# Optimization experiments

Measured on AMD Instinct MI355X. Metric: run time of the kernel, lower is better.

Reference implementation:

```python
import jax, jax.numpy as jnp
import numpy as np

B, S, NSAMP = 64, 21, 3000
HID, SEC, N, ATT = 500, 6, 2, 128
OUT, NPROTO, NCLS, NHEAD = 128, 25, 5, 4


def _pe(length, d):
    pos = np.arange(length, dtype=np.float32)[:, None]
    div = np.exp(np.arange(0, d, 2, dtype=np.float32) * (-np.log(10000.0) / d))
    pe = np.zeros((length, d), np.float32)
    pe[:, 0::2] = np.sin(pos * div)
    pe[:, 1::2] = np.cos(pos * div)
    return jnp.asarray(pe)


def _ln(x, g, b, eps=1e-5):
    m = x.mean(-1, keepdims=True)
    v = ((x - m) ** 2).mean(-1, keepdims=True)
    return (x - m) * jax.lax.rsqrt(v + eps) * g + b


def _conv1d(x, w, b):
    y = jax.lax.conv_general_dilated(x, w, (1,), [(1, 1)], dimension_numbers=('NCH', 'OIH', 'NCH'))
    return y + b[None, :, None]


def _maxpool(x, k):
    n, c, l = x.shape
    m = (l // k) * k  # torch MaxPool1d floors
    return x[:, :, :m].reshape(n, c, l // k, k).max(-1)


def _bn_eval(x, g, b, eps=1e-5):
    # eval-mode BatchNorm1d with running_mean=0, running_var=1
    return x * (g / np.sqrt(1.0 + eps))[None, :, None] + b[None, :, None]


def setup_inputs():
    key = jax.random.key(0)
    ks = jax.random.split(key, 16)
    def w(i, shape, s=0.02):
        return jax.random.normal(ks[i], shape, jnp.float32) * s
    u = jax.random.uniform(ks[0], (B * S * N, SEC), jnp.float32, 1e-6, 1.0 - 1e-6)
    return dict(
        x=jax.random.normal(ks[1], (B, S, 1, NSAMP), jnp.float32),
        gumbel=-jnp.log(-jnp.log(u)),
        wq=w(2, (HID, ATT * N)), wk=w(3, (HID, ATT * N)),
        w1=w(4, (32, 1, 3)), b1=jnp.zeros(32), bn1_g=jnp.ones(32), bn1_b=jnp.zeros(32),
        w2=w(5, (64, 32, 3)), b2=jnp.zeros(64), bn2_g=jnp.ones(64), bn2_b=jnp.zeros(64),
        w3=w(6, (128, 64, 3)), b3=jnp.zeros(128), bn3_g=jnp.ones(128), bn3_b=jnp.zeros(128),
        fc_w=w(7, (768, 256)), fc_b=jnp.zeros(256),
        fc2_w=w(8, (256, OUT)), fc2_b=jnp.zeros(OUT),
        protos=w(9, (NPROTO, OUT), 1.0),
        in_w=w(10, (OUT, 3 * OUT)), in_b=jnp.zeros(3 * OUT),
        out_w=w(11, (OUT, OUT)), out_b=jnp.zeros(OUT),
        ln1_g=jnp.ones(OUT), ln1_b=jnp.zeros(OUT),
        ln2_g=jnp.ones(OUT), ln2_b=jnp.zeros(OUT),
        ff1_w=w(12, (OUT, OUT)), ff1_b=jnp.zeros(OUT),
        ff2_w=w(13, (OUT, OUT)), ff2_b=jnp.zeros(OUT),
        clf_w=w(14, (OUT, NCLS)), clf_b=jnp.zeros(NCLS),
    )


def reference(x, gumbel, wq, wk, w1, b1, bn1_g, bn1_b, w2, b2, bn2_g, bn2_b,
              w3, b3, bn3_g, bn3_b, fc_w, fc_b, fc2_w, fc2_b, protos,
              in_w, in_b, out_w, out_b, ln1_g, ln1_b, ln2_g, ln2_b,
              ff1_w, ff1_b, ff2_w, ff2_b, clf_w, clf_b):
    bs = B * S
    # ---- HardAttentionLayer (gumbel hard sampling over SEC sections) ----
    xr = x.reshape(bs, SEC, HID)                       # (BS, 6, 500)
    xp = xr + _pe(100, HID)[None, :SEC]
    q = (xp @ wq).reshape(bs, SEC, N, ATT).transpose(0, 2, 1, 3)  # bnsh
    k = (xp @ wk).reshape(bs, SEC, N, ATT).transpose(0, 2, 1, 3)
    att = jnp.einsum('bnsh,bnth->bnst', q, k) / (HID ** 0.5)
    logits = (att.sum(-1) / SEC).reshape(bs * N, SEC)
    y_soft = jax.nn.softmax(logits + gumbel)           # tau = 1.0
    y_hard = jax.nn.one_hot(jnp.argmax(y_soft, -1), SEC, dtype=y_soft.dtype)
    alphas = (y_hard - jax.lax.stop_gradient(y_soft) + y_soft).reshape(bs, N, SEC)
    sampled = jnp.einsum('bns,bsh->bnh', alphas, xr)   # (BS, N, 500)
    # ---- conv/MLP epoch encoder (eval: dropout off, BN running stats) ----
    c = sampled.reshape(bs * N, 1, HID)
    c = _bn_eval(_maxpool(jax.nn.relu(_conv1d(c, w1, b1)), 4), bn1_g, bn1_b)
    c = _bn_eval(_maxpool(jax.nn.relu(_conv1d(c, w2, b2)), HID // 100), bn2_g, bn2_b)
    c = _bn_eval(_maxpool(jax.nn.relu(_conv1d(c, w3, b3)), 4), bn3_g, bn3_b)
    c = c.reshape(bs * N, -1) @ fc_w + fc_b
    z = c @ fc2_w + fc2_b                              # (B*S*N, 128)
    # ---- PrototypeLayer: VQ codebook lookup with straight-through ----
    d2 = (z * z).sum(1, keepdims=True) + (protos * protos).sum(1) - 2.0 * z @ protos.T
    proto = protos[jnp.argmin(d2, 1)]
    proto_st = z + jax.lax.stop_gradient(proto - z)
    # ---- SequenceEncoder: 1-layer post-norm transformer ----
    p_clf = proto_st.reshape(B, S, N, OUT).sum(2) / N  # (B, S, 128)
    h = p_clf + _pe(1024, OUT)[None, :S]
    qkv = h @ in_w + in_b
    qh, kh, vh = [t.reshape(B, S, NHEAD, OUT // NHEAD) for t in jnp.split(qkv, 3, -1)]
    sc = jnp.einsum('bqhd,bkhd->bhqk', qh, kh) / ((OUT // NHEAD) ** 0.5)
    ctx = jnp.einsum('bhqk,bkhd->bqhd', jax.nn.softmax(sc, -1), vh).reshape(B, S, OUT)
    h = _ln(h + ctx @ out_w + out_b, ln1_g, ln1_b)
    ff = jax.nn.relu(h @ ff1_w + ff1_b) @ ff2_w + ff2_b
    h = _ln(h + ff, ln2_g, ln2_b)
    return (h.reshape(-1, OUT) @ clf_w + clf_b).reshape(B, S, NCLS)
```

## Files before the change

kernel.cpp:

```cpp
#include <hip/hip_runtime.h>
#include <math.h>

#define BB 64
#define SS 21
#define NSAMP 3000
#define HID 500
#define SECN 6
#define NN 2
#define OUTD 128
#define NPROTO 25
#define NCLS 5
#define NHEAD 4
#define BS (BB*SS)
#define NSAMPLE (BS*NN)

#define C500 (-0.0184206807439523674f)
#define C128 (-0.07195578415606439f)
#define LSCALE 0.00745355992499929898f

#define WS_W2HI 5376
#define WS_W2LO 8448
#define WS_W3HI 11520
#define WS_W3LO 23808
#define WS_P3   36096
#define WS_C3   55296
#define WS_WQT  55424
#define WS_V    727424
#define WS_QKV  WS_V
#define WS_CTX  (WS_V + 520192)

typedef __attribute__((ext_vector_type(8))) short short8;
typedef __attribute__((ext_vector_type(4))) float floatx4;

__device__ __forceinline__ short f2bf(float f) {
  unsigned u = __float_as_uint(f);
  u += 0x7FFF + ((u >> 16) & 1);
  return (short)(u >> 16);
}
__device__ __forceinline__ float bf2f(short h) {
  return __uint_as_float(((unsigned)(unsigned short)h) << 16);
}

__global__ __launch_bounds__(256) void prep_all_kernel(
    const float* __restrict__ w2, const float* __restrict__ w3,
    short* __restrict__ w2hi, short* __restrict__ w2lo,
    short* __restrict__ w3hi, short* __restrict__ w3lo,
    const float* __restrict__ protos, const float* __restrict__ fc2w,
    const float* __restrict__ fcw, const float* __restrict__ fcb,
    const float* __restrict__ fc2b,
    float* __restrict__ P3, float* __restrict__ c3,
    const float* __restrict__ wq, float* __restrict__ wqT) {
  __shared__ __align__(16) float p2row[256];
  __shared__ float red[256];
  __shared__ float tile[64][65];
  const int t = threadIdx.x;
  if (blockIdx.x < 120) {
    int idx = blockIdx.x * 256 + t;
    if (idx < 6144) {
      int ic = idx & 31, ck = idx >> 5, k = ck % 3, c = ck / 3;
      float v = w2[c * 96 + ic * 3 + k];
      int dst = (((k * 4 + (c >> 4)) * 64) + ((ic >> 3) * 16 + (c & 15))) * 8 + (ic & 7);
      short hi = f2bf(v);
      short lo = f2bf(v - bf2f(hi));
      w2hi[dst] = hi; w2lo[dst] = lo;
    } else if (idx < 30720) {
      int j = idx - 6144;
      int ic = j & 63, ck = j >> 6, k = ck % 3, c = ck / 3;
      float v = w3[(c * 64 + ic) * 3 + k];
      int s = k * 2 + (ic >> 5);
      int dst = (((s * 8 + (c >> 4)) * 64) + (((ic & 31) >> 3) * 16 + (c & 15))) * 8 + (ic & 7);
      short hi = f2bf(v);
      short lo = f2bf(v - bf2f(hi));
      w3hi[dst] = hi; w3lo[dst] = lo;
    }
    return;
  }
  if (blockIdx.x >= 145) {
    int tid = blockIdx.x - 145;
    int h0 = (tid >> 2) * 64, c0 = (tid & 3) * 64;
    for (int e = t; e < 4096; e += 256) {
      int i = e >> 6, j = e & 63;
      if (h0 + i < 500) tile[j][i] = wq[(h0 + i) * 256 + c0 + j];
    }
    __syncthreads();
    for (int e = t; e < 4096; e += 256) {
      int c = e >> 6, hh = e & 63;
      if (h0 + hh < 500) wqT[(c0 + c) * 500 + h0 + hh] = tile[c][hh];
    }
    return;
  }
  const int p = blockIdx.x - 120, j = t;
  {
    const float4* pr = reinterpret_cast<const float4*>(protos + p * 128);
    const float4* wr = reinterpret_cast<const float4*>(fc2w + j * 128);
    float4 a4 = make_float4(0.f, 0.f, 0.f, 0.f);
    for (int c4 = 0; c4 < 32; c4++) {
      float4 a = pr[c4], b = wr[c4];
      a4.x += a.x * b.x; a4.y += a.y * b.y; a4.z += a.z * b.z; a4.w += a.w * b.w;
    }
    float v = (a4.x + a4.y) + (a4.z + a4.w);
    p2row[j] = v;
    float contrib = v * fcb[j];
    if (j < 128) {
      float pv = protos[p * 128 + j];
      contrib += pv * fc2b[j] - 0.5f * pv * pv;
    }
    red[j] = contrib;
  }
  __syncthreads();
  for (int s = 128; s > 0; s >>= 1) {
    if (j < s) red[j] += red[j + s];
    __syncthreads();
  }
  if (j == 0) c3[p] = red[0];
  for (int k = j; k < 768; k += 256) {
    const float4* fr = reinterpret_cast<const float4*>(fcw + k * 256);
    const float4* p2 = reinterpret_cast<const float4*>(p2row);
    float4 a4 = make_float4(0.f, 0.f, 0.f, 0.f);
    for (int j4 = 0; j4 < 64; j4++) {
      float4 a = p2[j4], b = fr[j4];
      a4.x += a.x * b.x; a4.y += a.y * b.y; a4.z += a.z * b.z; a4.w += a.w * b.w;
    }
    P3[p * 768 + k] = (a4.x + a4.y) + (a4.z + a4.w);
  }
}

#define MBX 4
__global__ __launch_bounds__(512) void attn_b_kernel(
    const float* __restrict__ x, const float* __restrict__ wk,
    const float* __restrict__ wqT, float* __restrict__ v) {
  __shared__ __align__(16) float pesum[500];
  __shared__ __align__(16) float xs[MBX * 500];
  __shared__ __align__(16) float ksp[2 * 256 * MBX];
  __shared__ __align__(16) float ks_t[256 * MBX];
  const int blk = blockIdx.x, t = threadIdx.x;

  if (t < 125) {
    float div0 = expf((float)(4 * t) * C500);
    float div1 = expf((float)(4 * t + 2) * C500);
    float s0 = 0.f, c0 = 0.f, s1 = 0.f, c1 = 0.f;
#pragma unroll
    for (int s = 0; s < SECN; s++) {
      float a0 = (float)s * div0, a1 = (float)s * div1;
      s0 += sinf(a0); c0 += cosf(a0);
      s1 += sinf(a1); c1 += cosf(a1);
    }
    reinterpret_cast<float4*>(pesum)[t] = make_float4(s0, c0, s1, c1);
  }
  __syncthreads();

  for (int e = t; e < MBX * 125; e += 512) {
    int m = e / 125, h4 = e % 125;
    const float4* xr = reinterpret_cast<const float4*>(x) + (blk * MBX + m) * 750;
    float4 a = xr[h4];
#pragma unroll
    for (int s = 1; s < SECN; s++) {
      float4 b = xr[s * 125 + h4];
      a.x += b.x; a.y += b.y; a.z += b.z; a.w += b.w;
    }
    float4 pe = reinterpret_cast<float4*>(pesum)[h4];
    a.x += pe.x; a.y += pe.y; a.z += pe.z; a.w += pe.w;
    reinterpret_cast<float4*>(xs)[m * 125 + h4] = a;
  }
  __syncthreads();

  {
    int c = t & 255, kh = t >> 8;
    float acc[MBX];
#pragma unroll
    for (int m = 0; m < MBX; m++) acc[m] = 0.f;
    int b4 = kh ? 63 : 0, e4 = kh ? 125 : 63;
    const float4* xsb = reinterpret_cast<const float4*>(xs);
    for (int i4 = b4; i4 < e4; i4++) {
      int i = i4 * 4;
      float w0 = wk[(i + 0) * 256 + c];
      float w1 = wk[(i + 1) * 256 + c];
      float w2 = wk[(i + 2) * 256 + c];
      float w3 = wk[(i + 3) * 256 + c];
#pragma unroll
      for (int m = 0; m < MBX; m++) {
        float4 xv = xsb[m * 125 + i4];
        acc[m] += xv.x * w0 + xv.y * w1 + xv.z * w2 + xv.w * w3;
      }
    }
#pragma unroll
    for (int m = 0; m < MBX; m++)
      ksp[(kh * 256 + c) * MBX + m] = acc[m];
  }
  __syncthreads();
  for (int e = t; e < 256 * MBX; e += 512) ks_t[e] = ksp[e] + ksp[256 * MBX + e];
  __syncthreads();

  if (t < 500) {
    int h = t;
#pragma unroll
    for (int n = 0; n < 2; n++) {
      float acc[MBX];
#pragma unroll
      for (int m = 0; m < MBX; m++) acc[m] = 0.f;
      const float* wcol = wqT + (n * 128) * 500 + h;
      const floatx4* ktb = (const floatx4*)ks_t + n * 128;
      for (int c = 0; c < 128; c++) {
        float w = wcol[c * 500];
        floatx4 k0 = ktb[c];
        acc[0] += w * k0[0]; acc[1] += w * k0[1]; acc[2] += w * k0[2]; acc[3] += w * k0[3];
      }
#pragma unroll
      for (int m = 0; m < MBX; m++)
        v[((blk * MBX + m) * 2 + n) * 500 + h] = acc[m];
    }
  }
}

__global__ __launch_bounds__(192) void attn_c_kernel(
    const float* __restrict__ x, const float* __restrict__ v,
    const float* __restrict__ gumbel, int* __restrict__ sec_idx) {
  __shared__ float lgsh[NN][SECN];
  const int bs = blockIdx.x, t = threadIdx.x;
  const int s = t >> 5, lane = t & 31;
  const float4* x4 = reinterpret_cast<const float4*>(x) + bs * 750 + s * 125;
  const float4* v0 = reinterpret_cast<const float4*>(v) + bs * 250;
  const float4* v1 = v0 + 125;
  float a0 = 0.f, a1 = 0.f;
  for (int h4 = lane; h4 < 125; h4 += 32) {
    float4 xv = x4[h4];
    float div0 = expf((float)(4 * h4) * C500);
    float div1 = expf((float)(4 * h4 + 2) * C500);
    float ang0 = (float)s * div0, ang1 = (float)s * div1;
    xv.x += sinf(ang0); xv.y += cosf(ang0);
    xv.z += sinf(ang1); xv.w += cosf(ang1);
    float4 w0 = v0[h4], w1 = v1[h4];
    a0 += xv.x * w0.x + xv.y * w0.y + xv.z * w0.z + xv.w * w0.w;
    a1 += xv.x * w1.x + xv.y * w1.y + xv.z * w1.z + xv.w * w1.w;
  }
#pragma unroll
  for (int m = 16; m >= 1; m >>= 1) {
    a0 += __shfl_xor(a0, m);
    a1 += __shfl_xor(a1, m);
  }
  if (lane == 0) {
    lgsh[0][s] = a0 * LSCALE + gumbel[(bs * 2 + 0) * SECN + s];
    lgsh[1][s] = a1 * LSCALE + gumbel[(bs * 2 + 1) * SECN + s];
  }
  __syncthreads();
  if (t < 2) {
    int best = 0; float bv = lgsh[t][0];
    for (int i = 1; i < SECN; i++) {
      float q = lgsh[t][i];
      if (q > bv) { bv = q; best = i; }
    }
    sec_idx[bs * 2 + t] = best;
  }
}

#define CONV_LDS 53568
__global__ __launch_bounds__(512, 6) void conv_kernel(
    const float* __restrict__ x, const int* __restrict__ sec_idx,
    const float* __restrict__ w1, const float* __restrict__ b1,
    const float* __restrict__ bn1g, const float* __restrict__ bn1b,
    const short* __restrict__ w2hi, const short* __restrict__ w2lo,
    const float* __restrict__ b2,
    const float* __restrict__ bn2g, const float* __restrict__ bn2b,
    const short* __restrict__ w3hi, const short* __restrict__ w3lo,
    const float* __restrict__ b3,
    const float* __restrict__ bn3g, const float* __restrict__ bn3b,
    const float* __restrict__ P3, const float* __restrict__ c3,
    int* __restrict__ proto_idx) {
  __shared__ __align__(16) char smem[CONV_LDS];
  short* act1_hi  = (short*)smem;
  short* act1_lo  = (short*)(smem + 10400);
  short* act2p_hi = (short*)smem;
  short* act2p_lo = (short*)(smem + 4896);
  float* featsh   = (float*)(smem + 9792);
  float* sc25     = (float*)(smem + 12864);
  float* in0p  = (float*)(smem + 20800);
  float* act2t = (float*)(smem + 20800);
  float* act3t = (float*)(smem + 20800);

  const int sample = blockIdx.x;
  const int t = threadIdx.x;
  const int bsIdx = sample >> 1;
  const float bnscale = rsqrtf(1.0f + 1e-5f);
  const int wv = t >> 6, l = t & 63, lr = l & 15, lg2 = l >> 4;

  {
    int sec = sec_idx[sample];
    const float* src = &x[bsIdx * NSAMP + sec * HID];
    if (t < 512) in0p[t] = (t >= 1 && t <= 500) ? src[t - 1] : 0.f;
    if (t < 200) {
      int r = t / 40; r = (r == 0) ? 0 : 125 + r;
      int idx = r * 40 + t % 40;
      act1_hi[idx] = 0; act1_lo[idx] = 0;
    }
  }
  __syncthreads();

  {
    int ic = t & 31;
    float w0 = w1[ic * 3], w1v = w1[ic * 3 + 1], w2v = w1[ic * 3 + 2];
    float bb = b1[ic];
    float g = bn1g[ic] * bnscale, be = bn1b[ic];
    for (int p = t >> 5; p < 125; p += 16) {
      int base = 4 * p;
      float xm1 = in0p[base], x0 = in0p[base + 1], x1 = in0p[base + 2],
            x2 = in0p[base + 3], x3 = in0p[base + 4], x4 = in0p[base + 5];
      float a0 = bb + w0 * xm1 + w1v * x0 + w2v * x1;
      float a1 = bb + w0 * x0  + w1v * x1 + w2v * x2;
      float a2 = bb + w0 * x1  + w1v * x2 + w2v * x3;
      float a3 = bb + w0 * x2  + w1v * x3 + w2v * x4;
      float m = fmaxf(fmaxf(fmaxf(fmaxf(a0, a1), a2), a3), 0.f);
      float v = m * g + be;
      short hi = f2bf(v);
      short lo = f2bf(v - bf2f(hi));
      act1_hi[(p + 1) * 40 + ic] = hi;
      act1_lo[(p + 1) * 40 + ic] = lo;
    }
  }
  __syncthreads();

  {
    floatx4 acc[4];
#pragma unroll
    for (int m = 0; m < 4; m++) acc[m] = (floatx4){0.f, 0.f, 0.f, 0.f};
#pragma unroll
    for (int s = 0; s < 3; s++) {
      short8 Ah[4], Al[4], Bh, Bl;
#pragma unroll
      for (int m = 0; m < 4; m++) {
        int aoff = ((s * 4 + m) * 64 + l) * 8;
        Ah[m] = *(const short8*)(w2hi + aoff);
        Al[m] = *(const short8*)(w2lo + aoff);
      }
      {
        int boff = (wv * 16 + lr + s) * 40 + lg2 * 8;
        Bh = *(const short8*)(act1_hi + boff);
        Bl = *(const short8*)(act1_lo + boff);
      }
#pragma unroll
      for (int m = 0; m < 4; m++) {
        acc[m] = __builtin_amdgcn_mfma_f32_16x16x32_bf16(Ah[m], Bh, acc[m], 0, 0, 0);
        acc[m] = __builtin_amdgcn_mfma_f32_16x16x32_bf16(Ah[m], Bl, acc[m], 0, 0, 0);
        acc[m] = __builtin_amdgcn_mfma_f32_16x16x32_bf16(Al[m], Bh, acc[m], 0, 0, 0);
      }
    }
#pragma unroll
    for (int m = 0; m < 4; m++) {
      int p = wv * 16 + lr;
      int swz = (m * 4 + lg2) ^ lr;
      *(floatx4*)(act2t + p * 64 + swz * 4) = acc[m];
    }
  }
  __syncthreads();

  {
    if (t < 162) {
      for (int i = t; i < 648; i += 162) {
        int r = i / 72; r = (r == 0) ? 0 : 25 + r;
        int idx = r * 72 + i % 72;
        act2p_hi[idx] = 0; act2p_lo[idx] = 0;
      }
    }
    int ic = t & 63;
    float bb = b2[ic], g = bn2g[ic] * bnscale, be = bn2b[ic];
#define A2T(r, c) act2t[(r) * 64 + ((((c) >> 2) ^ ((r) & 15)) << 2) + ((c) & 3)]
    for (int pw = t >> 6; pw < 25; pw += 8) {
      int base = 5 * pw;
      float m = A2T(base, ic);
      m = fmaxf(m, A2T(base + 1, ic));
      m = fmaxf(m, A2T(base + 2, ic));
      m = fmaxf(m, A2T(base + 3, ic));
      m = fmaxf(m, A2T(base + 4, ic));
      float v = fmaxf(m + bb, 0.f) * g + be;
      short hi = f2bf(v);
      short lo = f2bf(v - bf2f(hi));
      act2p_hi[(pw + 1) * 72 + ic] = hi;
      act2p_lo[(pw + 1) * 72 + ic] = lo;
    }
#undef A2T
  }
  __syncthreads();

  {
    floatx4 acc[2];
#pragma unroll
    for (int nn = 0; nn < 2; nn++) acc[nn] = (floatx4){0.f, 0.f, 0.f, 0.f};
#pragma unroll
    for (int s = 0; s < 6; s++) {
      short8 Ah, Al, Bh[2], Bl[2];
      {
        int aoff = ((s * 8 + wv) * 64 + l) * 8;
        Ah = *(const short8*)(w3hi + aoff);
        Al = *(const short8*)(w3lo + aoff);
      }
#pragma unroll
      for (int nn = 0; nn < 2; nn++) {
        int boff = (nn * 16 + lr + (s >> 1)) * 72 + (s & 1) * 32 + lg2 * 8;
        Bh[nn] = *(const short8*)(act2p_hi + boff);
        Bl[nn] = *(const short8*)(act2p_lo + boff);
      }
#pragma unroll
      for (int nn = 0; nn < 2; nn++) {
        acc[nn] = __builtin_amdgcn_mfma_f32_16x16x32_bf16(Ah, Bh[nn], acc[nn], 0, 0, 0);
        acc[nn] = __builtin_amdgcn_mfma_f32_16x16x32_bf16(Ah, Bl[nn], acc[nn], 0, 0, 0);
        acc[nn] = __builtin_amdgcn_mfma_f32_16x16x32_bf16(Al, Bh[nn], acc[nn], 0, 0, 0);
      }
    }
#pragma unroll
    for (int nn = 0; nn < 2; nn++) {
      int p = nn * 16 + lr;
      *(floatx4*)(act3t + p * 132 + wv * 16 + lg2 * 4) = acc[nn];
    }
  }
  __syncthreads();

  {
    int c = t & 127;
    float bb = b3[c], g = bn3g[c] * bnscale, be = bn3b[c];
    for (int pw = t >> 7; pw < 6; pw += 4) {
      int base = 4 * pw;
      float m = act3t[base * 132 + c];
      m = fmaxf(m, act3t[(base + 1) * 132 + c]);
      m = fmaxf(m, act3t[(base + 2) * 132 + c]);
      m = fmaxf(m, act3t[(base + 3) * 132 + c]);
      float v = fmaxf(m + bb, 0.f) * g + be;
      featsh[c * 6 + pw] = v;
    }
  }
  __syncthreads();

  if (t < NPROTO * 8) {
    int p = t >> 3, part = t & 7;
    const float4* pr = reinterpret_cast<const float4*>(P3 + p * 768 + part * 96);
    const float4* fr = reinterpret_cast<const float4*>(featsh + part * 96);
    float4 a4 = make_float4(0.f, 0.f, 0.f, 0.f);
#pragma unroll
    for (int i = 0; i < 24; i++) {
      float4 w = pr[i], f = fr[i];
      a4.x += w.x * f.x; a4.y += w.y * f.y; a4.z += w.z * f.z; a4.w += w.w * f.w;
    }
    float a = (a4.x + a4.y) + (a4.z + a4.w);
    a += __shfl_xor(a, 1);
    a += __shfl_xor(a, 2);
    a += __shfl_xor(a, 4);
    if (part == 0) sc25[p] = a + c3[p];
  }
  __syncthreads();
  if (t == 0) {
    int best = 0; float bv = sc25[0];
    for (int i = 1; i < NPROTO; i++) {
      float v = sc25[i];
      if (v > bv) { bv = v; best = i; }
    }
    proto_idx[sample] = best;
  }
}

__global__ __launch_bounds__(384) void seq_qkv_kernel(
    const int* __restrict__ proto_idx, const float* __restrict__ protos,
    const float* __restrict__ inw, const float* __restrict__ inb,
    float* __restrict__ qkv) {
  __shared__ __align__(16) float hrow[OUTD];
  const int bs = blockIdx.x, t = threadIdx.x;
  const int s = bs % SS;
  if (t < OUTD) {
    int i0 = proto_idx[bs * 2], i1 = proto_idx[bs * 2 + 1];
    float pc = 0.5f * (protos[i0 * OUTD + t] + protos[i1 * OUTD + t]);
    float div = expf((float)(2 * (t >> 1)) * C128);
    float ang = (float)s * div;
    float pe = (t & 1) ? cosf(ang) : sinf(ang);
    hrow[t] = pc + pe;
  }
  __syncthreads();
  float a = inb[t];
  const float4* hr = reinterpret_cast<const float4*>(hrow);
  for (int d4 = 0; d4 < 32; d4++) {
    float4 h4 = hr[d4];
    int d = d4 * 4;
    a += h4.x * inw[(d + 0) * 384 + t] + h4.y * inw[(d + 1) * 384 + t]
       + h4.z * inw[(d + 2) * 384 + t] + h4.w * inw[(d + 3) * 384 + t];
  }
  qkv[bs * 384 + t] = a;
}

__global__ __launch_bounds__(256) void seq_attn_kernel(
    const float* __restrict__ qkv, float* __restrict__ ctxbuf) {
  __shared__ float qs_[SS][32], ks_[SS][32], vs_[SS][32];
  __shared__ float sc_[SS][SS + 1];
  const int b = blockIdx.x >> 2, hd = blockIdx.x & 3;
  const int t = threadIdx.x;
  for (int e = t; e < SS * 32; e += 256) {
    int s = e >> 5, dd = e & 31;
    const float* base = qkv + (b * SS + s) * 384 + hd * 32 + dd;
    qs_[s][dd] = base[0];
    ks_[s][dd] = base[128];
    vs_[s][dd] = base[256];
  }
  __syncthreads();
  for (int e = t; e < SS * SS; e += 256) {
    int qs = e / SS, ks = e % SS;
    float a = 0.f;
#pragma unroll
    for (int d = 0; d < 32; d++) a += qs_[qs][d] * ks_[ks][d];
    sc_[qs][ks] = a * 0.17677669529663689f;
  }
  __syncthreads();
  if (t < SS) {
    float mx = sc_[t][0];
    for (int i = 1; i < SS; i++) mx = fmaxf(mx, sc_[t][i]);
    float sum = 0.f;
    for (int i = 0; i < SS; i++) { float e = expf(sc_[t][i] - mx); sc_[t][i] = e; sum += e; }
    float inv = 1.f / sum;
    for (int i = 0; i < SS; i++) sc_[t][i] *= inv;
  }
  __syncthreads();
  for (int e = t; e < SS * 32; e += 256) {
    int qs = e >> 5, dd = e & 31;
    float a = 0.f;
#pragma unroll
    for (int ks = 0; ks < SS; ks++) a += sc_[qs][ks] * vs_[ks][dd];
    ctxbuf[(b * SS + qs) * OUTD + hd * 32 + dd] = a;
  }
}

__global__ __launch_bounds__(128) void seq_tail_kernel(
    const int* __restrict__ proto_idx, const float* __restrict__ protos,
    const float* __restrict__ ctxbuf,
    const float* __restrict__ outw, const float* __restrict__ outb,
    const float* __restrict__ ln1g, const float* __restrict__ ln1b,
    const float* __restrict__ ff1w, const float* __restrict__ ff1b,
    const float* __restrict__ ff2w, const float* __restrict__ ff2b,
    const float* __restrict__ ln2g, const float* __restrict__ ln2b,
    const float* __restrict__ clfw, const float* __restrict__ clfb,
    float* __restrict__ out) {
  __shared__ __align__(16) float rowA[OUTD];
  __shared__ __align__(16) float rowB[OUTD];
  __shared__ float lds2[2];
  const int bs = blockIdx.x, t = threadIdx.x;
  const int s = bs % SS;

  rowA[t] = ctxbuf[bs * OUTD + t];
  __syncthreads();
  float a = outb[t];
  {
    const float4* cr = reinterpret_cast<const float4*>(rowA);
    for (int e4 = 0; e4 < 32; e4++) {
      float4 c4 = cr[e4];
      int e = e4 * 4;
      a += c4.x * outw[(e + 0) * OUTD + t] + c4.y * outw[(e + 1) * OUTD + t]
         + c4.z * outw[(e + 2) * OUTD + t] + c4.w * outw[(e + 3) * OUTD + t];
    }
  }
  float hv;
  {
    int i0 = proto_idx[bs * 2], i1 = proto_idx[bs * 2 + 1];
    float pc = 0.5f * (protos[i0 * OUTD + t] + protos[i1 * OUTD + t]);
    float div = expf((float)(2 * (t >> 1)) * C128);
    float ang = (float)s * div;
    float pe = (t & 1) ? cosf(ang) : sinf(ang);
    hv = pc + pe;
  }
  float tmp = hv + a;
  {
    float v = tmp;
#pragma unroll
    for (int k = 32; k >= 1; k >>= 1) v += __shfl_xor(v, k);
    if ((t & 63) == 0) lds2[t >> 6] = v;
    __syncthreads();
    float m = (lds2[0] + lds2[1]) * (1.0f / OUTD);
    __syncthreads();
    float u = tmp - m;
    float w = u * u;
#pragma unroll
    for (int k = 32; k >= 1; k >>= 1) w += __shfl_xor(w, k);
    if ((t & 63) == 0) lds2[t >> 6] = w;
    __syncthreads();
    float var = (lds2[0] + lds2[1]) * (1.0f / OUTD);
    __syncthreads();
    rowA[t] = u * rsqrtf(var + 1e-5f) * ln1g[t] + ln1b[t];
  }
  __syncthreads();
  {
    float r = ff1b[t];
    const float4* hr = reinterpret_cast<const float4*>(rowA);
    for (int e4 = 0; e4 < 32; e4++) {
      float4 h4 = hr[e4];
      int e = e4 * 4;
      r += h4.x * ff1w[(e + 0) * OUTD + t] + h4.y * ff1w[(e + 1) * OUTD + t]
         + h4.z * ff1w[(e + 2) * OUTD + t] + h4.w * ff1w[(e + 3) * OUTD + t];
    }
    rowB[t] = fmaxf(r, 0.f);
  }
  __syncthreads();
  float tmp2;
  {
    float r = ff2b[t];
    const float4* cr = reinterpret_cast<const float4*>(rowB);
    for (int e4 = 0; e4 < 32; e4++) {
      float4 c4 = cr[e4];
      int e = e4 * 4;
      r += c4.x * ff2w[(e + 0) * OUTD + t] + c4.y * ff2w[(e + 1) * OUTD + t]
         + c4.z * ff2w[(e + 2) * OUTD + t] + c4.w * ff2w[(e + 3) * OUTD + t];
    }
    tmp2 = rowA[t] + r;
  }
  __syncthreads();
  {
    float v = tmp2;
#pragma unroll
    for (int k = 32; k >= 1; k >>= 1) v += __shfl_xor(v, k);
    if ((t & 63) == 0) lds2[t >> 6] = v;
    __syncthreads();
    float m = (lds2[0] + lds2[1]) * (1.0f / OUTD);
    __syncthreads();
    float u = tmp2 - m;
    float w = u * u;
#pragma unroll
    for (int k = 32; k >= 1; k >>= 1) w += __shfl_xor(w, k);
    if ((t & 63) == 0) lds2[t >> 6] = w;
    __syncthreads();
    float var = (lds2[0] + lds2[1]) * (1.0f / OUTD);
    rowA[t] = u * rsqrtf(var + 1e-5f) * ln2g[t] + ln2b[t];
  }
  __syncthreads();
  if (t < NCLS) {
    float acc = clfb[t];
    for (int d = 0; d < OUTD; d++) acc += rowA[d] * clfw[d * NCLS + t];
    out[bs * NCLS + t] = acc;
  }
}

extern "C" void kernel_launch(void* const* d_in, const int* in_sizes, int n_in,
                              void* d_out, int out_size, void* d_ws, size_t ws_size,
                              hipStream_t stream) {
  const float* x     = (const float*)d_in[0];
  const float* gum   = (const float*)d_in[1];
  const float* wq    = (const float*)d_in[2];
  const float* wk    = (const float*)d_in[3];
  const float* w1    = (const float*)d_in[4];
  const float* b1    = (const float*)d_in[5];
  const float* bn1g  = (const float*)d_in[6];
  const float* bn1b  = (const float*)d_in[7];
  const float* w2    = (const float*)d_in[8];
  const float* b2    = (const float*)d_in[9];
  const float* bn2g  = (const float*)d_in[10];
  const float* bn2b  = (const float*)d_in[11];
  const float* w3    = (const float*)d_in[12];
  const float* b3    = (const float*)d_in[13];
  const float* bn3g  = (const float*)d_in[14];
  const float* bn3b  = (const float*)d_in[15];
  const float* fcw   = (const float*)d_in[16];
  const float* fcb   = (const float*)d_in[17];
  const float* fc2w  = (const float*)d_in[18];
  const float* fc2b  = (const float*)d_in[19];
  const float* prot  = (const float*)d_in[20];
  const float* inw   = (const float*)d_in[21];
  const float* inb   = (const float*)d_in[22];
  const float* outw  = (const float*)d_in[23];
  const float* outb  = (const float*)d_in[24];
  const float* ln1g  = (const float*)d_in[25];
  const float* ln1b  = (const float*)d_in[26];
  const float* ln2g  = (const float*)d_in[27];
  const float* ln2b  = (const float*)d_in[28];
  const float* ff1w  = (const float*)d_in[29];
  const float* ff1b  = (const float*)d_in[30];
  const float* ff2w  = (const float*)d_in[31];
  const float* ff2b  = (const float*)d_in[32];
  const float* clfw  = (const float*)d_in[33];
  const float* clfb  = (const float*)d_in[34];
  float* out = (float*)d_out;

  int* sec_idx   = (int*)d_ws;
  int* proto_idx = sec_idx + NSAMPLE;
  short* w2hi = (short*)((float*)d_ws + WS_W2HI);
  short* w2lo = (short*)((float*)d_ws + WS_W2LO);
  short* w3hi = (short*)((float*)d_ws + WS_W3HI);
  short* w3lo = (short*)((float*)d_ws + WS_W3LO);
  float* P3   = (float*)d_ws + WS_P3;
  float* c3   = (float*)d_ws + WS_C3;
  float* wqT  = (float*)d_ws + WS_WQT;
  float* vbuf = (float*)d_ws + WS_V;
  float* qkv  = (float*)d_ws + WS_QKV;
  float* ctxb = (float*)d_ws + WS_CTX;

  hipLaunchKernelGGL(prep_all_kernel, dim3(177), dim3(256), 0, stream,
                     w2, w3, w2hi, w2lo, w3hi, w3lo,
                     prot, fc2w, fcw, fcb, fc2b, P3, c3, wq, wqT);
  hipLaunchKernelGGL(attn_b_kernel, dim3(BS / MBX), dim3(512), 0, stream,
                     x, wk, wqT, vbuf);
  hipLaunchKernelGGL(attn_c_kernel, dim3(BS), dim3(192), 0, stream,
                     x, vbuf, gum, sec_idx);
  hipLaunchKernelGGL(conv_kernel, dim3(NSAMPLE), dim3(512), 0, stream,
                     x, sec_idx, w1, b1, bn1g, bn1b, w2hi, w2lo, b2, bn2g, bn2b,
                     w3hi, w3lo, b3, bn3g, bn3b, P3, c3, proto_idx);
  hipLaunchKernelGGL(seq_qkv_kernel, dim3(BS), dim3(384), 0, stream,
                     proto_idx, prot, inw, inb, qkv);
  hipLaunchKernelGGL(seq_attn_kernel, dim3(BB * NHEAD), dim3(256), 0, stream,
                     qkv, ctxb);
  hipLaunchKernelGGL(seq_tail_kernel, dim3(BS), dim3(128), 0, stream,
                     proto_idx, prot, ctxb, outw, outb, ln1g, ln1b,
                     ff1w, ff1b, ff2w, ff2b, ln2g, ln2b, clfw, clfb, out);
}
```

Baseline: 183.1 us.

## Restructure kernel pipeline: fuse prep into attention, fuse QKV into seq attention, repad conv LDS

The weight prep and prototype-projection work moves into the attention-scoring kernel as extra blocks, with only the wq transpose kept as its own small launch. The sequence QKV projection is fused into the per-head attention kernel, so the qkv buffer round trip and one launch go away, though each head block recomputes its whole h row. The conv kernel's act2 LDS row stride changes from 72 to 68 shorts to reduce bank conflicts, and 8-wide loads are split into pairs of 4-wide loads. Its occupancy hint in launch bounds drops from 6 to 3, which may raise register use per thread.

```diff
diff --git a/kernel.cpp b/kernel.cpp
--- a/kernel.cpp
+++ b/kernel.cpp
@@ -26,10 +26,10 @@
 #define WS_C3   55296
 #define WS_WQT  55424
 #define WS_V    727424
-#define WS_QKV  WS_V
 #define WS_CTX  (WS_V + 520192)
 
 typedef __attribute__((ext_vector_type(8))) short short8;
+typedef __attribute__((ext_vector_type(4))) short short4v;
 typedef __attribute__((ext_vector_type(4))) float floatx4;
 
 __device__ __forceinline__ short f2bf(float f) {
@@ -41,99 +41,103 @@
   return __uint_as_float(((unsigned)(unsigned short)h) << 16);
 }
 
-__global__ __launch_bounds__(256) void prep_all_kernel(
+__global__ __launch_bounds__(256) void transpose_kernel(
+    const float* __restrict__ wq, float* __restrict__ wqT) {
+  __shared__ float tile[64][65];
+  const int t = threadIdx.x;
+  int h0 = (blockIdx.x >> 2) * 64, c0 = (blockIdx.x & 3) * 64;
+  for (int e = t; e < 4096; e += 256) {
+    int i = e >> 6, j = e & 63;
+    if (h0 + i < 500) tile[j][i] = wq[(h0 + i) * 256 + c0 + j];
+  }
+  __syncthreads();
+  for (int e = t; e < 4096; e += 256) {
+    int c = e >> 6, hh = e & 63;
+    if (h0 + hh < 500) wqT[(c0 + c) * 500 + h0 + hh] = tile[c][hh];
+  }
+}
+
+#define MBX 4
+__global__ __launch_bounds__(512) void attn_prep_kernel(
+    const float* __restrict__ x, const float* __restrict__ wk,
+    const float* __restrict__ wqT, float* __restrict__ v,
     const float* __restrict__ w2, const float* __restrict__ w3,
     short* __restrict__ w2hi, short* __restrict__ w2lo,
     short* __restrict__ w3hi, short* __restrict__ w3lo,
     const float* __restrict__ protos, const float* __restrict__ fc2w,
     const float* __restrict__ fcw, const float* __restrict__ fcb,
     const float* __restrict__ fc2b,
-    float* __restrict__ P3, float* __restrict__ c3,
-    const float* __restrict__ wq, float* __restrict__ wqT) {
-  __shared__ __align__(16) float p2row[256];
-  __shared__ float red[256];
-  __shared__ float tile[64][65];
+    float* __restrict__ P3, float* __restrict__ c3) {
   const int t = threadIdx.x;
-  if (blockIdx.x < 120) {
-    int idx = blockIdx.x * 256 + t;
-    if (idx < 6144) {
-      int ic = idx & 31, ck = idx >> 5, k = ck % 3, c = ck / 3;
-      float v = w2[c * 96 + ic * 3 + k];
-      int dst = (((k * 4 + (c >> 4)) * 64) + ((ic >> 3) * 16 + (c & 15))) * 8 + (ic & 7);
-      short hi = f2bf(v);
-      short lo = f2bf(v - bf2f(hi));
-      w2hi[dst] = hi; w2lo[dst] = lo;
-    } else if (idx < 30720) {
-      int j = idx - 6144;
-      int ic = j & 63, ck = j >> 6, k = ck % 3, c = ck / 3;
-      float v = w3[(c * 64 + ic) * 3 + k];
-      int s = k * 2 + (ic >> 5);
-      int dst = (((s * 8 + (c >> 4)) * 64) + (((ic & 31) >> 3) * 16 + (c & 15))) * 8 + (ic & 7);
-      short hi = f2bf(v);
-      short lo = f2bf(v - bf2f(hi));
-      w3hi[dst] = hi; w3lo[dst] = lo;
+  if (blockIdx.x >= 336) {
+    int pid = blockIdx.x - 336;
+    if (pid < 120) {
+      if (t < 256) {
+        int idx = pid * 256 + t;
+        if (idx < 6144) {
+          int ic = idx & 31, ck = idx >> 5, k = ck % 3, c = ck / 3;
+          float vv = w2[c * 96 + ic * 3 + k];
+          int dst = (((k * 4 + (c >> 4)) * 64) + ((ic >> 3) * 16 + (c & 15))) * 8 + (ic & 7);
+          short hi = f2bf(vv);
+          short lo = f2bf(vv - bf2f(hi));
+          w2hi[dst] = hi; w2lo[dst] = lo;
+        } else if (idx < 30720) {
+          int j = idx - 6144;
+          int ic = j & 63, ck = j >> 6, k = ck % 3, c = ck / 3;
+          float vv = w3[(c * 64 + ic) * 3 + k];
+          int s = k * 2 + (ic >> 5);
+          int dst = (((s * 8 + (c >> 4)) * 64) + (((ic & 31) >> 3) * 16 + (c & 15))) * 8 + (ic & 7);
+          short hi = f2bf(vv);
+          short lo = f2bf(vv - bf2f(hi));
+          w3hi[dst] = hi; w3lo[dst] = lo;
+        }
+      }
+      return;
+    }
+    __shared__ __align__(16) float p2row[256];
+    __shared__ float red[256];
+    const int p = pid - 120, j = t;
+    if (j < 256) {
+      const float4* pr = reinterpret_cast<const float4*>(protos + p * 128);
+      const float4* wr = reinterpret_cast<const float4*>(fc2w + j * 128);
+      float4 a4 = make_float4(0.f, 0.f, 0.f, 0.f);
+      for (int c4 = 0; c4 < 32; c4++) {
+        float4 a = pr[c4], b = wr[c4];
+        a4.x += a.x * b.x; a4.y += a.y * b.y; a4.z += a.z * b.z; a4.w += a.w * b.w;
+      }
+      float vv = (a4.x + a4.y) + (a4.z + a4.w);
+      p2row[j] = vv;
+      float contrib = vv * fcb[j];
+      if (j < 128) {
+        float pv = protos[p * 128 + j];
+        contrib += pv * fc2b[j] - 0.5f * pv * pv;
+      }
+      red[j] = contrib;
+    }
+    __syncthreads();
+    for (int s = 128; s > 0; s >>= 1) {
+      if (j < s) red[j] += red[j + s];
+      __syncthreads();
+    }
+    if (j == 0) c3[p] = red[0];
+    for (int k = t; k < 768; k += 512) {
+      const float4* fr = reinterpret_cast<const float4*>(fcw + k * 256);
+      const float4* p2 = reinterpret_cast<const float4*>(p2row);
+      float4 a4 = make_float4(0.f, 0.f, 0.f, 0.f);
+      for (int j4 = 0; j4 < 64; j4++) {
+        float4 a = p2[j4], b = fr[j4];
+        a4.x += a.x * b.x; a4.y += a.y * b.y; a4.z += a.z * b.z; a4.w += a.w * b.w;
+      }
+      P3[p * 768 + k] = (a4.x + a4.y) + (a4.z + a4.w);
     }
     return;
   }
-  if (blockIdx.x >= 145) {
-    int tid = blockIdx.x - 145;
-    int h0 = (tid >> 2) * 64, c0 = (tid & 3) * 64;
-    for (int e = t; e < 4096; e += 256) {
-      int i = e >> 6, j = e & 63;
-      if (h0 + i < 500) tile[j][i] = wq[(h0 + i) * 256 + c0 + j];
-    }
-    __syncthreads();
-    for (int e = t; e < 4096; e += 256) {
-      int c = e >> 6, hh = e & 63;
-      if (h0 + hh < 500) wqT[(c0 + c) * 500 + h0 + hh] = tile[c][hh];
-    }
-    return;
-  }
-  const int p = blockIdx.x - 120, j = t;
-  {
-    const float4* pr = reinterpret_cast<const float4*>(protos + p * 128);
-    const float4* wr = reinterpret_cast<const float4*>(fc2w + j * 128);
-    float4 a4 = make_float4(0.f, 0.f, 0.f, 0.f);
-    for (int c4 = 0; c4 < 32; c4++) {
-      float4 a = pr[c4], b = wr[c4];
-      a4.x += a.x * b.x; a4.y += a.y * b.y; a4.z += a.z * b.z; a4.w += a.w * b.w;
-    }
-    float v = (a4.x + a4.y) + (a4.z + a4.w);
-    p2row[j] = v;
-    float contrib = v * fcb[j];
-    if (j < 128) {
-      float pv = protos[p * 128 + j];
-      contrib += pv * fc2b[j] - 0.5f * pv * pv;
-    }
-    red[j] = contrib;
-  }
-  __syncthreads();
-  for (int s = 128; s > 0; s >>= 1) {
-    if (j < s) red[j] += red[j + s];
-    __syncthreads();
-  }
-  if (j == 0) c3[p] = red[0];
-  for (int k = j; k < 768; k += 256) {
-    const float4* fr = reinterpret_cast<const float4*>(fcw + k * 256);
-    const float4* p2 = reinterpret_cast<const float4*>(p2row);
-    float4 a4 = make_float4(0.f, 0.f, 0.f, 0.f);
-    for (int j4 = 0; j4 < 64; j4++) {
-      float4 a = p2[j4], b = fr[j4];
-      a4.x += a.x * b.x; a4.y += a.y * b.y; a4.z += a.z * b.z; a4.w += a.w * b.w;
-    }
-    P3[p * 768 + k] = (a4.x + a4.y) + (a4.z + a4.w);
-  }
-}
-
-#define MBX 4
-__global__ __launch_bounds__(512) void attn_b_kernel(
-    const float* __restrict__ x, const float* __restrict__ wk,
-    const float* __restrict__ wqT, float* __restrict__ v) {
+
   __shared__ __align__(16) float pesum[500];
   __shared__ __align__(16) float xs[MBX * 500];
   __shared__ __align__(16) float ksp[2 * 256 * MBX];
   __shared__ __align__(16) float ks_t[256 * MBX];
-  const int blk = blockIdx.x, t = threadIdx.x;
+  const int blk = blockIdx.x;
 
   if (t < 125) {
     float div0 = expf((float)(4 * t) * C500);
@@ -175,12 +179,12 @@
       int i = i4 * 4;
       float w0 = wk[(i + 0) * 256 + c];
       float w1 = wk[(i + 1) * 256 + c];
-      float w2 = wk[(i + 2) * 256 + c];
-      float w3 = wk[(i + 3) * 256 + c];
+      float w2v = wk[(i + 2) * 256 + c];
+      float w3v = wk[(i + 3) * 256 + c];
 #pragma unroll
       for (int m = 0; m < MBX; m++) {
         float4 xv = xsb[m * 125 + i4];
-        acc[m] += xv.x * w0 + xv.y * w1 + xv.z * w2 + xv.w * w3;
+        acc[m] += xv.x * w0 + xv.y * w1 + xv.z * w2v + xv.w * w3v;
       }
     }
 #pragma unroll
@@ -254,7 +258,8 @@
 }
 
 #define CONV_LDS 53568
-__global__ __launch_bounds__(512, 6) void conv_kernel(
+#define ST2P 68
+__global__ __launch_bounds__(512, 3) void conv_kernel(
     const float* __restrict__ x, const int* __restrict__ sec_idx,
     const float* __restrict__ w1, const float* __restrict__ b1,
     const float* __restrict__ bn1g, const float* __restrict__ bn1b,
@@ -270,7 +275,7 @@
   short* act1_hi  = (short*)smem;
   short* act1_lo  = (short*)(smem + 10400);
   short* act2p_hi = (short*)smem;
-  short* act2p_lo = (short*)(smem + 4896);
+  short* act2p_lo = (short*)(smem + 4624);
   float* featsh   = (float*)(smem + 9792);
   float* sc25     = (float*)(smem + 12864);
   float* in0p  = (float*)(smem + 20800);
@@ -353,10 +358,10 @@
   __syncthreads();
 
   {
-    if (t < 162) {
-      for (int i = t; i < 648; i += 162) {
-        int r = i / 72; r = (r == 0) ? 0 : 25 + r;
-        int idx = r * 72 + i % 72;
+    if (t < 153) {
+      for (int i = t; i < 612; i += 153) {
+        int r = i / ST2P; r = (r == 0) ? 0 : 25 + r;
+        int idx = r * ST2P + i % ST2P;
         act2p_hi[idx] = 0; act2p_lo[idx] = 0;
       }
     }
@@ -373,8 +378,8 @@
       float v = fmaxf(m + bb, 0.f) * g + be;
       short hi = f2bf(v);
       short lo = f2bf(v - bf2f(hi));
-      act2p_hi[(pw + 1) * 72 + ic] = hi;
-      act2p_lo[(pw + 1) * 72 + ic] = lo;
+      act2p_hi[(pw + 1) * ST2P + ic] = hi;
+      act2p_lo[(pw + 1) * ST2P + ic] = lo;
     }
 #undef A2T
   }
@@ -394,9 +399,13 @@
       }
 #pragma unroll
       for (int nn = 0; nn < 2; nn++) {
-        int boff = (nn * 16 + lr + (s >> 1)) * 72 + (s & 1) * 32 + lg2 * 8;
-        Bh[nn] = *(const short8*)(act2p_hi + boff);
-        Bl[nn] = *(const short8*)(act2p_lo + boff);
+        int boff = (nn * 16 + lr + (s >> 1)) * ST2P + (s & 1) * 32 + lg2 * 8;
+        short4v h0 = *(const short4v*)(act2p_hi + boff);
+        short4v h1 = *(const short4v*)(act2p_hi + boff + 4);
+        short4v l0 = *(const short4v*)(act2p_lo + boff);
+        short4v l1 = *(const short4v*)(act2p_lo + boff + 4);
+        Bh[nn] = (short8){h0[0], h0[1], h0[2], h0[3], h1[0], h1[1], h1[2], h1[3]};
+        Bl[nn] = (short8){l0[0], l0[1], l0[2], l0[3], l1[0], l1[1], l1[2], l1[3]};
       }
 #pragma unroll
       for (int nn = 0; nn < 2; nn++) {
@@ -455,47 +464,46 @@
   }
 }
 
-__global__ __launch_bounds__(384) void seq_qkv_kernel(
+__global__ __launch_bounds__(256) void seq_qk_attn_kernel(
     const int* __restrict__ proto_idx, const float* __restrict__ protos,
     const float* __restrict__ inw, const float* __restrict__ inb,
-    float* __restrict__ qkv) {
-  __shared__ __align__(16) float hrow[OUTD];
-  const int bs = blockIdx.x, t = threadIdx.x;
-  const int s = bs % SS;
-  if (t < OUTD) {
-    int i0 = proto_idx[bs * 2], i1 = proto_idx[bs * 2 + 1];
-    float pc = 0.5f * (protos[i0 * OUTD + t] + protos[i1 * OUTD + t]);
-    float div = expf((float)(2 * (t >> 1)) * C128);
-    float ang = (float)s * div;
-    float pe = (t & 1) ? cosf(ang) : sinf(ang);
-    hrow[t] = pc + pe;
-  }
-  __syncthreads();
-  float a = inb[t];
-  const float4* hr = reinterpret_cast<const float4*>(hrow);
-  for (int d4 = 0; d4 < 32; d4++) {
-    float4 h4 = hr[d4];
-    int d = d4 * 4;
-    a += h4.x * inw[(d + 0) * 384 + t] + h4.y * inw[(d + 1) * 384 + t]
-       + h4.z * inw[(d + 2) * 384 + t] + h4.w * inw[(d + 3) * 384 + t];
-  }
-  qkv[bs * 384 + t] = a;
-}
-
-__global__ __launch_bounds__(256) void seq_attn_kernel(
-    const float* __restrict__ qkv, float* __restrict__ ctxbuf) {
+    float* __restrict__ ctxbuf) {
+  __shared__ __align__(16) float hsh[SS * OUTD];
   __shared__ float qs_[SS][32], ks_[SS][32], vs_[SS][32];
   __shared__ float sc_[SS][SS + 1];
   const int b = blockIdx.x >> 2, hd = blockIdx.x & 3;
   const int t = threadIdx.x;
-  for (int e = t; e < SS * 32; e += 256) {
-    int s = e >> 5, dd = e & 31;
-    const float* base = qkv + (b * SS + s) * 384 + hd * 32 + dd;
-    qs_[s][dd] = base[0];
-    ks_[s][dd] = base[128];
-    vs_[s][dd] = base[256];
-  }
-  __syncthreads();
+
+  for (int o = t; o < SS * OUTD; o += 256) {
+    int s = o >> 7, d = o & 127;
+    int i0 = proto_idx[(b * SS + s) * 2];
+    int i1 = proto_idx[(b * SS + s) * 2 + 1];
+    float pc = 0.5f * (protos[i0 * OUTD + d] + protos[i1 * OUTD + d]);
+    float div = expf((float)(2 * (d >> 1)) * C128);
+    float ang = (float)s * div;
+    float pe = (d & 1) ? cosf(ang) : sinf(ang);
+    hsh[o] = pc + pe;
+  }
+  __syncthreads();
+
+  for (int o = t; o < SS * 96; o += 256) {
+    int s = o / 96, j = o % 96;
+    int sec = j >> 5, dd = j & 31;
+    int col = sec * 128 + hd * 32 + dd;
+    float a = inb[col];
+    const float4* hr = reinterpret_cast<const float4*>(&hsh[s * OUTD]);
+    for (int d4 = 0; d4 < 32; d4++) {
+      float4 h4 = hr[d4];
+      int d = d4 * 4;
+      a += h4.x * inw[(d + 0) * 384 + col] + h4.y * inw[(d + 1) * 384 + col]
+         + h4.z * inw[(d + 2) * 384 + col] + h4.w * inw[(d + 3) * 384 + col];
+    }
+    if (sec == 0) qs_[s][dd] = a;
+    else if (sec == 1) ks_[s][dd] = a;
+    else vs_[s][dd] = a;
+  }
+  __syncthreads();
+
   for (int e = t; e < SS * SS; e += 256) {
     int qs = e / SS, ks = e % SS;
     float a = 0.f;
@@ -679,23 +687,20 @@
   float* c3   = (float*)d_ws + WS_C3;
   float* wqT  = (float*)d_ws + WS_WQT;
   float* vbuf = (float*)d_ws + WS_V;
-  float* qkv  = (float*)d_ws + WS_QKV;
   float* ctxb = (float*)d_ws + WS_CTX;
 
-  hipLaunchKernelGGL(prep_all_kernel, dim3(177), dim3(256), 0, stream,
+  hipLaunchKernelGGL(transpose_kernel, dim3(32), dim3(256), 0, stream, wq, wqT);
+  hipLaunchKernelGGL(attn_prep_kernel, dim3(336 + 145), dim3(512), 0, stream,
+                     x, wk, wqT, vbuf,
                      w2, w3, w2hi, w2lo, w3hi, w3lo,
-                     prot, fc2w, fcw, fcb, fc2b, P3, c3, wq, wqT);
-  hipLaunchKernelGGL(attn_b_kernel, dim3(BS / MBX), dim3(512), 0, stream,
-                     x, wk, wqT, vbuf);
+                     prot, fc2w, fcw, fcb, fc2b, P3, c3);
   hipLaunchKernelGGL(attn_c_kernel, dim3(BS), dim3(192), 0, stream,
                      x, vbuf, gum, sec_idx);
   hipLaunchKernelGGL(conv_kernel, dim3(NSAMPLE), dim3(512), 0, stream,
                      x, sec_idx, w1, b1, bn1g, bn1b, w2hi, w2lo, b2, bn2g, bn2b,
                      w3hi, w3lo, b3, bn3g, bn3b, P3, c3, proto_idx);
-  hipLaunchKernelGGL(seq_qkv_kernel, dim3(BS), dim3(384), 0, stream,
-                     proto_idx, prot, inw, inb, qkv);
-  hipLaunchKernelGGL(seq_attn_kernel, dim3(BB * NHEAD), dim3(256), 0, stream,
-                     qkv, ctxb);
+  hipLaunchKernelGGL(seq_qk_attn_kernel, dim3(BB * NHEAD), dim3(256), 0, stream,
+                     proto_idx, prot, inw, inb, ctxb);
   hipLaunchKernelGGL(seq_tail_kernel, dim3(BS), dim3(128), 0, stream,
                      proto_idx, prot, ctxb, outw, outb, ln1g, ln1b,
                      ff1w, ff1b, ff2w, ff2b, ln2g, ln2b, clfw, clfb, out);
```

Result: slower. 191.9 us (+4.8%).
